# Kernel tuning notes

Measured on AMD Instinct MI355X. Metric: run time of the kernel, lower is better.

Reference implementation:

```python
import jax, jax.numpy as jnp
import numpy as np

ATTN_SPLITS = 2
TEMPERATURE = 10000.0

# ---------- split / merge helpers (faithful to split_feature / merge_splits) ----------

def split_cf(x, ns):  # channel-first [b,c,h,w] -> [b*ns*ns, c, h/ns, w/ns]
    b, c, h, w = x.shape
    x = x.reshape(b, c, ns, h // ns, ns, w // ns).transpose(0, 2, 4, 1, 3, 5)
    return x.reshape(b * ns * ns, c, h // ns, w // ns)

def merge_cf(x, ns):  # channel-first inverse
    b, c, h, w = x.shape
    nb = b // (ns * ns)
    x = x.reshape(nb, ns, ns, c, h, w).transpose(0, 3, 1, 4, 2, 5)
    return x.reshape(nb, c, ns * h, ns * w)

def split_cl(x, ns):  # channel-last [b,h,w,c] -> [b*ns*ns, h/ns, w/ns, c]
    b, h, w, c = x.shape
    x = x.reshape(b, ns, h // ns, ns, w // ns, c).transpose(0, 1, 3, 2, 4, 5)
    return x.reshape(b * ns * ns, h // ns, w // ns, c)

def merge_cl(x, ns):  # channel-last inverse
    b, h, w, c = x.shape
    nb = b // (ns * ns)
    x = x.reshape(nb, ns, ns, h, w, c).transpose(0, 1, 3, 2, 4, 5)
    return x.reshape(nb, ns * h, ns * w, c)

# ---------- PositionEmbeddingSine (normalize=True, scale=2*pi) ----------

def pos_embed_sine(h, w, num_pos_feats):
    scale = 2.0 * np.pi
    eps = 1e-6
    ones = jnp.ones((h, w), jnp.float32)
    y_embed = jnp.cumsum(ones, 0)
    x_embed = jnp.cumsum(ones, 1)
    y_embed = y_embed / (y_embed[-1:, :] + eps) * scale
    x_embed = x_embed / (x_embed[:, -1:] + eps) * scale
    dim_t = jnp.arange(num_pos_feats, dtype=jnp.float32)
    dim_t = TEMPERATURE ** (2.0 * jnp.floor(dim_t / 2.0) / num_pos_feats)
    pos_x = x_embed[:, :, None] / dim_t  # [h,w,npf]
    pos_y = y_embed[:, :, None] / dim_t
    pos_x = jnp.stack([jnp.sin(pos_x[:, :, 0::2]), jnp.cos(pos_x[:, :, 1::2])], -1).reshape(h, w, -1)
    pos_y = jnp.stack([jnp.sin(pos_y[:, :, 0::2]), jnp.cos(pos_y[:, :, 1::2])], -1).reshape(h, w, -1)
    pos = jnp.concatenate([pos_y, pos_x], -1)  # [h,w,c]
    return jnp.transpose(pos, (2, 0, 1))[None]  # [1,c,h,w]

def feature_add_position(f0, f1, attn_splits, c):
    if attn_splits > 1:
        f0s = split_cf(f0, attn_splits)
        f1s = split_cf(f1, attn_splits)
        pos = pos_embed_sine(f0s.shape[2], f0s.shape[3], c // 2)
        return merge_cf(f0s + pos, attn_splits), merge_cf(f1s + pos, attn_splits)
    pos = pos_embed_sine(f0.shape[2], f0.shape[3], c // 2)
    return f0 + pos, f1 + pos

# ---------- shifted-window attention mask (static, numpy) ----------

def shift_window_attn_mask(h, w, ns):
    wsh, wsw = h // ns, w // ns
    ssh, ssw = wsh // 2, wsw // 2
    img = np.zeros((h, w), np.float32)
    cnt = 0
    for hs in (slice(0, -wsh), slice(-wsh, -ssh), slice(-ssh, None)):
        for ws in (slice(0, -wsw), slice(-wsw, -ssw), slice(-ssw, None)):
            img[hs, ws] = cnt
            cnt += 1
    m = img.reshape(ns, wsh, ns, wsw).transpose(0, 2, 1, 3).reshape(ns * ns, wsh * wsw)
    am = m[:, None, :] - m[:, :, None]
    am = np.where(am != 0, -100.0, 0.0).astype(np.float32)
    return jnp.asarray(am)  # [ns*ns, N, N]

# ---------- single-head split (shifted) window attention ----------

def split_window_attention(q, k, v, ns, h, w, attn_mask):
    b, _, c = q.shape
    bn = b * ns * ns
    wsh, wsw = h // ns, w // ns
    ssh, ssw = wsh // 2, wsw // 2
    q = q.reshape(b, h, w, c)
    k = k.reshape(b, h, w, c)
    v = v.reshape(b, h, w, c)
    q = jnp.roll(q, (-ssh, -ssw), (1, 2))
    k = jnp.roll(k, (-ssh, -ssw), (1, 2))
    v = jnp.roll(v, (-ssh, -ssw), (1, 2))
    qs = split_cl(q, ns).reshape(bn, -1, c)
    ks = split_cl(k, ns).reshape(bn, -1, c)
    vs = split_cl(v, ns).reshape(bn, -1, c)
    scores = jnp.einsum('bnc,bmc->bnm', qs, ks) / jnp.sqrt(jnp.asarray(c, qs.dtype))
    scores = scores + jnp.tile(attn_mask, (b, 1, 1))
    attn = jax.nn.softmax(scores, axis=-1)
    out = jnp.einsum('bnm,bmc->bnc', attn, vs)
    out = merge_cl(out.reshape(bn, wsh, wsw, c), ns)
    out = jnp.roll(out, (ssh, ssw), (1, 2))
    return out.reshape(b, -1, c)

# ---------- global correlation softmax matching ----------

def global_correlation_softmax(f0, f1):
    b, c, h, w = f0.shape
    f0v = f0.reshape(b, c, -1)  # [b,c,hw]
    f1v = f1.reshape(b, c, -1)
    corr = jnp.einsum('bcn,bcm->bnm', f0v, f1v) / jnp.sqrt(jnp.asarray(c, f0.dtype))
    yy, xx = jnp.meshgrid(jnp.arange(h), jnp.arange(w), indexing='ij')
    grid = jnp.stack([xx, yy], 0).astype(f0.dtype)  # [2,h,w] (x,y)
    gridv = grid.reshape(2, -1).T  # [hw,2]
    prob = jax.nn.softmax(corr, axis=-1)
    corresp = jnp.einsum('bnm,md->bnd', prob, gridv).reshape(b, h, w, 2).transpose(0, 3, 1, 2)
    flow = corresp - grid[None]
    return flow

# ---------- setup & reference ----------

def setup_inputs() -> dict:
    key = jax.random.key(0)
    k0, k1 = jax.random.split(key)
    b, c, h, w = 4, 128, 64, 64
    feature0 = jax.random.normal(k0, (b, c, h, w), jnp.float32)
    feature1 = jax.random.normal(k1, (b, c, h, w), jnp.float32)
    return {'feature0': feature0, 'feature1': feature1}

def reference(feature0, feature1):
    b, c, h, w = feature0.shape
    ns = ATTN_SPLITS
    f0, f1 = feature_add_position(feature0, feature1, ns, c)
    attn_mask = shift_window_attn_mask(h, w, ns)
    q = f0.reshape(b, c, -1).transpose(0, 2, 1)  # [b,hw,c]
    kv = f1.reshape(b, c, -1).transpose(0, 2, 1)
    f0_attn = split_window_attention(q, kv, kv, ns, h, w, attn_mask)  # [b,hw,c]
    f0_attn = f0_attn.transpose(0, 2, 1).reshape(b, c, h, w)
    flow = global_correlation_softmax(f0_attn, f1)  # [b,2,h,w]
    return flow
```

## Files before the change

### kernel.cpp

```cpp
#include <hip/hip_runtime.h>
#include <hip/hip_bf16.h>
#include <math.h>

#define NB 4
#define NC 128
#define NH 64
#define NW 64
#define NHW 4096
#define SCALE 0.08838834764831845f

typedef short bf16x8 __attribute__((ext_vector_type(8)));
typedef float f32x4 __attribute__((ext_vector_type(4)));

__device__ __forceinline__ unsigned bfbits(float f) {
    unsigned u = __float_as_uint(f);
    return (u + 0x7FFFu + ((u >> 16) & 1u)) >> 16;
}
__device__ __forceinline__ unsigned bfpair(float a, float b) {
    return bfbits(a) | (bfbits(b) << 16);
}

__global__ __launch_bounds__(256) void pos_kernel(float* __restrict__ pos) {
    int idx = blockIdx.x * 256 + threadIdx.x;
    if (idx >= NC * 32 * 32) return;
    int x = idx & 31;
    int y = (idx >> 5) & 31;
    int c = idx >> 10;
    const float twopi = 6.283185307179586f;
    const float denom = 32.0f + 1e-6f;
    int cc = (c < 64) ? c : (c - 64);
    float e = (c < 64) ? (float)(y + 1) : (float)(x + 1);
    e = e * (twopi / denom);
    int k = cc >> 1;
    float arg = e * exp2f(-0.41524101186091903f * (float)k);
    pos[idx] = (cc & 1) ? cosf(arg) : sinf(arg);
}

__global__ __launch_bounds__(256) void pack_kernel(
        const float* __restrict__ f0, const float* __restrict__ f1,
        const float* __restrict__ pos,
        __hip_bfloat16* __restrict__ Qw, __hip_bfloat16* __restrict__ Kw,
        __hip_bfloat16* __restrict__ Bt, __hip_bfloat16* __restrict__ Ktw) {
    __shared__ float T[64][129];
    int blk = blockIdx.x;
    const bool isA = blk < 256;
    const float* src = isA ? f0 : f1;
    blk &= 255;
    const int y = blk & 63;
    const int b = blk >> 6;
    const int tid = threadIdx.x;
    const float* s = src + (size_t)b * NC * NHW + y * 64;
    for (int idx = tid; idx < 64 * NC; idx += 256) {
        const int x = idx & 63, c = idx >> 6;
        T[x][c] = s[c * NHW + x] + pos[(c << 10) + ((y & 31) << 5) + (x & 31)];
    }
    __syncthreads();
    const float sA = isA ? SCALE : 1.0f;
    const int yp = (y + 48) & 63;
    const int wi = yp >> 5, ry = yp & 31;
    for (int idx = tid; idx < 512; idx += 256) {
        const int x = idx >> 3, c0 = (idx & 7) * 16;
        const int xp = (x + 48) & 63;
        const int wj = xp >> 5, rx = xp & 31;
        const int win = b * 4 + wi * 2 + wj;
        const int tok = ry * 32 + rx;
        const float* tr = &T[x][c0];
        uint4 v0, v1;
        v0.x = bfpair(tr[0] * sA, tr[1] * sA);   v0.y = bfpair(tr[2] * sA, tr[3] * sA);
        v0.z = bfpair(tr[4] * sA, tr[5] * sA);   v0.w = bfpair(tr[6] * sA, tr[7] * sA);
        v1.x = bfpair(tr[8] * sA, tr[9] * sA);   v1.y = bfpair(tr[10] * sA, tr[11] * sA);
        v1.z = bfpair(tr[12] * sA, tr[13] * sA); v1.w = bfpair(tr[14] * sA, tr[15] * sA);
        __hip_bfloat16* wrow = (isA ? Qw : Kw) + ((size_t)win * 1024 + tok) * NC + c0;
        *reinterpret_cast<uint4*>(wrow) = v0;
        *reinterpret_cast<uint4*>(wrow + 8) = v1;
        if (!isA) {
            __hip_bfloat16* brow = Bt + ((size_t)b * NHW + y * 64 + x) * NC + c0;
            *reinterpret_cast<uint4*>(brow) = v0;
            *reinterpret_cast<uint4*>(brow + 8) = v1;
        }
    }
    if (!isA) {
        const int c = tid >> 1;
        const int wj = tid & 1;
        const int win = b * 4 + wi * 2 + wj;
        unsigned up[16];
        #pragma unroll
        for (int pr = 0; pr < 16; ++pr) {
            const int x0 = ((wj << 5) + 2 * pr + 16) & 63;
            up[pr] = bfpair(T[x0][c], T[x0 + 1][c]);
        }
        __hip_bfloat16* krow = Ktw + ((size_t)win * NC + c) * 1024 + ry * 32;
        uint4* uv = reinterpret_cast<uint4*>(up);
        #pragma unroll
        for (int i = 0; i < 4; ++i)
            *reinterpret_cast<uint4*>(krow + i * 8) = uv[i];
    }
}

__global__ __launch_bounds__(256) void attn_mfma_kernel(
        const __hip_bfloat16* __restrict__ Qw,
        const __hip_bfloat16* __restrict__ Kw,
        const __hip_bfloat16* __restrict__ Ktw,
        __hip_bfloat16* __restrict__ At) {
    __shared__ __align__(16) char lds[73728];
    char* KsB = lds;
    char* VsB = lds + 32768;
    char* Pscr = lds + 65536;
    const int tid = threadIdx.x;
    const int lane = tid & 63;
    const int w = tid >> 6;
    const int l15 = lane & 15;
    const int g = lane >> 4;
    const int blk = blockIdx.x;
    const int win = blk >> 4;
    const int qt = blk & 15;
    const int b = win >> 2, wi = (win >> 1) & 1, wj = win & 1;

    const char* Ksrc = (const char*)(Kw + (size_t)win * 1024 * NC);
    const char* Vsrc = (const char*)(Ktw + (size_t)win * NC * 1024);

    bf16x8 qf[4];
    {
        const __hip_bfloat16* qrow =
            Qw + ((size_t)win * 1024 + qt * 64 + w * 16 + l15) * NC + g * 8;
        #pragma unroll
        for (int kk = 0; kk < 4; ++kk)
            qf[kk] = *reinterpret_cast<const bf16x8*>(qrow + kk * 32);
    }

    const int reg_q = (wi ? (qt < 8 ? 1 : 2) : 0) * 3
                    + (wj ? ((w & 1) == 0 ? 1 : 2) : 0);

    auto stageK = [&](int buf, int kt) {
        const char* sb = Ksrc + (size_t)kt * 64 * 256;
        char* dst = KsB + buf * 16384;
        #pragma unroll
        for (int it = 0; it < 4; ++it) {
            const int obase = w * 4096 + it * 1024;
            const int o = obase + lane * 16;
            const int row = o >> 8;
            const int off = o & 255;
            __builtin_amdgcn_global_load_lds(
                (const __attribute__((address_space(1))) void*)(sb + row * 256 + (off ^ ((row & 7) << 4))),
                (__attribute__((address_space(3))) void*)(dst + obase), 16, 0, 0);
        }
    };
    auto stageV = [&](int buf, int kt) {
        char* dst = VsB + buf * 16384;
        #pragma unroll
        for (int it = 0; it < 4; ++it) {
            const int obase = w * 4096 + it * 1024;
            const int o = obase + lane * 16;
            const int crow = o >> 7;
            const int off = o & 127;
            __builtin_amdgcn_global_load_lds(
                (const __attribute__((address_space(1))) void*)(Vsrc + crow * 2048 + kt * 128 + (off ^ ((crow & 7) << 4))),
                (__attribute__((address_space(3))) void*)(dst + obase), 16, 0, 0);
        }
    };

    f32x4 oacc[8] = {{0,0,0,0},{0,0,0,0},{0,0,0,0},{0,0,0,0},
                     {0,0,0,0},{0,0,0,0},{0,0,0,0},{0,0,0,0}};
    float zacc = 0.f;

    stageK(0, 0); stageV(0, 0);
    __syncthreads();

    for (int kt = 0; kt < 16; ++kt) {
        const int buf = kt & 1;
        if (kt < 15) { stageK(buf ^ 1, kt + 1); stageV(buf ^ 1, kt + 1); }

        const char* kb = KsB + buf * 16384;
        f32x4 sacc[4] = {{0,0,0,0},{0,0,0,0},{0,0,0,0},{0,0,0,0}};
        #pragma unroll
        for (int kk = 0; kk < 4; ++kk) {
            #pragma unroll
            for (int msub = 0; msub < 4; ++msub) {
                const int byte = msub * 4096 + l15 * 256 + ((kk * 64 + g * 16) ^ ((l15 & 7) << 4));
                bf16x8 kf = *reinterpret_cast<const bf16x8*>(kb + byte);
                sacc[msub] = __builtin_amdgcn_mfma_f32_16x16x32_bf16(kf, qf[kk], sacc[msub], 0, 0, 0);
            }
        }

        const int rk_row = (wi ? (kt < 8 ? 1 : 2) : 0) * 3;
        char* pw = Pscr + w * 2048;
        #pragma unroll
        for (int msub = 0; msub < 4; ++msub) {
            const int rk = rk_row + (wj ? ((msub & 1) == 0 ? 1 : 2) : 0);
            const bool ok = (rk == reg_q);
            const float p0 = ok ? __expf(sacc[msub][0]) : 0.f;
            const float p1 = ok ? __expf(sacc[msub][1]) : 0.f;
            const float p2 = ok ? __expf(sacc[msub][2]) : 0.f;
            const float p3 = ok ? __expf(sacc[msub][3]) : 0.f;
            zacc += (p0 + p1) + (p2 + p3);
            *reinterpret_cast<unsigned*>(pw + l15 * 128 + ((msub * 32 + g * 8 + 0) ^ ((l15 & 7) << 4))) = bfpair(p0, p1);
            *reinterpret_cast<unsigned*>(pw + l15 * 128 + ((msub * 32 + g * 8 + 4) ^ ((l15 & 7) << 4))) = bfpair(p2, p3);
        }
        bf16x8 pf[2];
        #pragma unroll
        for (int kk = 0; kk < 2; ++kk)
            pf[kk] = *reinterpret_cast<const bf16x8*>(pw + l15 * 128 + ((kk * 64 + g * 16) ^ ((l15 & 7) << 4)));

        const char* vb = VsB + buf * 16384;
        #pragma unroll
        for (int kk = 0; kk < 2; ++kk) {
            #pragma unroll
            for (int co = 0; co < 8; ++co) {
                const int byte = (co * 16 + l15) * 128 + ((kk * 64 + g * 16) ^ ((l15 & 7) << 4));
                bf16x8 vf = *reinterpret_cast<const bf16x8*>(vb + byte);
                oacc[co] = __builtin_amdgcn_mfma_f32_16x16x32_bf16(pf[kk], vf, oacc[co], 0, 0, 0);
            }
        }
        __syncthreads();
    }

    float z = zacc;
    z += __shfl_xor(z, 16);
    z += __shfl_xor(z, 32);

    unsigned short* olds = reinterpret_cast<unsigned short*>(lds + w * 4096);
    #pragma unroll
    for (int r = 0; r < 4; ++r) {
        const float zi = SCALE / __shfl(z, g * 4 + r);
        #pragma unroll
        for (int co = 0; co < 8; ++co)
            olds[(g * 4 + r) * 128 + co * 16 + l15] = (unsigned short)bfbits(oacc[co][r] * zi);
    }

    const int qloc = lane >> 2;
    const int c0 = (lane & 3) * 32;
    const int tok = qt * 64 + w * 16 + qloc;
    const int yo = ((wi << 5) + (tok >> 5) + 16) & 63;
    const int xo = ((wj << 5) + (tok & 31) + 16) & 63;
    __hip_bfloat16* arow = At + ((size_t)b * NHW + yo * 64 + xo) * NC + c0;
    #pragma unroll
    for (int i = 0; i < 4; ++i) {
        int4 v = *reinterpret_cast<const int4*>(olds + qloc * 128 + c0 + i * 8);
        *reinterpret_cast<int4*>(arow + i * 8) = v;
    }
}

__global__ __launch_bounds__(256) void corr_part_kernel(
        const __hip_bfloat16* __restrict__ At,
        const __hip_bfloat16* __restrict__ Bt,
        float4* __restrict__ part) {
    __shared__ __hip_bfloat16 Bs[2][64 * 128];
    const int tid = threadIdx.x;
    const int lane = tid & 63;
    const int w = tid >> 6;
    const int blk = blockIdx.x;
    const int ms = blk & 3;
    const int nt = (blk >> 2) & 63;
    const int b = blk >> 8;
    const int l15 = lane & 15;
    const int g = lane >> 4;
    const int n0 = nt * 64;

    const __hip_bfloat16* Ab = At + (size_t)b * NHW * NC;
    const __hip_bfloat16* Bb = Bt + (size_t)b * NHW * NC;

    bf16x8 afrag[4];
    {
        const __hip_bfloat16* arow = Ab + (size_t)(n0 + w * 16 + l15) * NC + g * 8;
        #pragma unroll
        for (int kk = 0; kk < 4; ++kk)
            afrag[kk] = *reinterpret_cast<const bf16x8*>(arow + kk * 32);
    }

    auto stage = [&](int buf, int mtile) {
        const char* srcbase = reinterpret_cast<const char*>(Bb + (size_t)mtile * 64 * NC);
        #pragma unroll
        for (int it = 0; it < 4; ++it) {
            const int obase = w * 4096 + it * 1024;
            const int o = obase + lane * 16;
            const int row = o >> 8;
            const int off = o & 255;
            const char* src = srcbase + row * 256 + (off ^ ((row & 7) << 4));
            __builtin_amdgcn_global_load_lds(
                (const __attribute__((address_space(1))) void*)src,
                (__attribute__((address_space(3))) void*)((char*)&Bs[buf][0] + obase),
                16, 0, 0);
        }
    };

    f32x4 rl = {0, 0, 0, 0}, rsm = {0, 0, 0, 0}, rsy = {0, 0, 0, 0};

    stage(0, ms * 16);
    __syncthreads();

    for (int mt = 0; mt < 16; ++mt) {
        const int buf = mt & 1;
        if (mt < 15) stage(buf ^ 1, ms * 16 + mt + 1);

        f32x4 acc[4] = {{0,0,0,0},{0,0,0,0},{0,0,0,0},{0,0,0,0}};
        const char* base = (const char*)&Bs[buf][0];
        #pragma unroll
        for (int kk = 0; kk < 4; ++kk) {
            #pragma unroll
            for (int msub = 0; msub < 4; ++msub) {
                const int byte = msub * 4096 + l15 * 256 +
                                 ((kk * 64 + g * 16) ^ ((l15 & 7) << 4));
                bf16x8 bfrag = *reinterpret_cast<const bf16x8*>(base + byte);
                acc[msub] = __builtin_amdgcn_mfma_f32_16x16x32_bf16(
                    afrag[kk], bfrag, acc[msub], 0, 0, 0);
            }
        }
        const float y0 = (float)(ms * 16 + mt);
        #pragma unroll
        for (int r = 0; r < 4; ++r) {
            float p0 = __expf(acc[0][r]);
            float p1 = __expf(acc[1][r]);
            float p2 = __expf(acc[2][r]);
            float p3 = __expf(acc[3][r]);
            float ts = (p0 + p1) + (p2 + p3);
            rl[r]  += ts;
            rsy[r] += y0 * ts;
            rsm[r] += fmaf(3.f, p3, fmaf(2.f, p2, p1));
        }
        __syncthreads();
    }

    const float xl = (float)l15;
    #pragma unroll
    for (int r = 0; r < 4; ++r) {
        float a  = rl[r];
        float sx = xl * rl[r] + 16.f * rsm[r];
        float sy = rsy[r];
        #pragma unroll
        for (int m = 1; m < 16; m <<= 1) {
            a  += __shfl_xor(a, m);
            sx += __shfl_xor(sx, m);
            sy += __shfl_xor(sy, m);
        }
        if (l15 == 0) {
            const int n = n0 + w * 16 + g * 4 + r;
            part[((size_t)b * NHW + n) * 4 + ms] = make_float4(a, sx, sy, 0.f);
        }
    }
}

__global__ __launch_bounds__(256) void finalize_kernel(
        const float4* __restrict__ part, float* __restrict__ out) {
    const int idx = blockIdx.x * 256 + threadIdx.x;
    if (idx >= NB * NHW) return;
    const int n = idx & (NHW - 1);
    const int b = idx >> 12;
    float4 p0 = part[(size_t)idx * 4 + 0];
    float4 p1 = part[(size_t)idx * 4 + 1];
    float4 p2 = part[(size_t)idx * 4 + 2];
    float4 p3 = part[(size_t)idx * 4 + 3];
    const float l  = (p0.x + p1.x) + (p2.x + p3.x);
    const float sx = (p0.y + p1.y) + (p2.y + p3.y);
    const float sy = (p0.z + p1.z) + (p2.z + p3.z);
    const float inv = 1.0f / l;
    out[(size_t)b * 2 * NHW + n]       = sx * inv - (float)(n & 63);
    out[(size_t)b * 2 * NHW + NHW + n] = sy * inv - (float)(n >> 6);
}

extern "C" void kernel_launch(void* const* d_in, const int* in_sizes, int n_in,
                              void* d_out, int out_size, void* d_ws, size_t ws_size,
                              hipStream_t stream) {
    const float* f0 = (const float*)d_in[0];
    const float* f1 = (const float*)d_in[1];
    float* ws  = (float*)d_ws;
    float* pos = ws;
    __hip_bfloat16* Qw  = (__hip_bfloat16*)(pos + 131072);
    __hip_bfloat16* Kw  = Qw  + (size_t)16 * 1024 * NC;
    __hip_bfloat16* Bt  = Kw  + (size_t)16 * 1024 * NC;
    __hip_bfloat16* Ktw = Bt  + (size_t)NB * NHW * NC;
    __hip_bfloat16* At  = Ktw + (size_t)16 * NC * 1024;
    float4* part = (float4*)(At + (size_t)NB * NHW * NC);
    float* out = (float*)d_out;

    pos_kernel<<<512, 256, 0, stream>>>(pos);
    pack_kernel<<<512, 256, 0, stream>>>(f0, f1, pos, Qw, Kw, Bt, Ktw);
    attn_mfma_kernel<<<256, 256, 0, stream>>>(Qw, Kw, Ktw, At);
    corr_part_kernel<<<1024, 256, 0, stream>>>(At, Bt, part);
    finalize_kernel<<<64, 256, 0, stream>>>(part, out);
}
```

Before: 70.12 us.

## Inline position embedding, drop windowed Q/K copies, reshape correlation tiling

The separate position-embedding kernel is removed and sin/cos is computed inline in the pack kernel. The windowed, shifted Q and K buffers are no longer written; the attention kernel gathers Q and K rows directly from the plain row-major layouts using shifted-window index math, which saves one launch and two full bf16 copies. The correlation kernel now gives each wave 32 query rows sharing the staged B tile, with 8 M-splits instead of 4, and finalize sums 8 partials. This trades extra transcendental work in pack and scattered K loads for less global traffic and more reuse of each B tile.

Measured after the change: 74.75 us. +6.6%, slower.

```diff
diff --git a/kernel.cpp b/kernel.cpp
--- a/kernel.cpp
+++ b/kernel.cpp
@@ -20,27 +20,19 @@
     return bfbits(a) | (bfbits(b) << 16);
 }
 
-__global__ __launch_bounds__(256) void pos_kernel(float* __restrict__ pos) {
-    int idx = blockIdx.x * 256 + threadIdx.x;
-    if (idx >= NC * 32 * 32) return;
-    int x = idx & 31;
-    int y = (idx >> 5) & 31;
-    int c = idx >> 10;
-    const float twopi = 6.283185307179586f;
-    const float denom = 32.0f + 1e-6f;
-    int cc = (c < 64) ? c : (c - 64);
-    float e = (c < 64) ? (float)(y + 1) : (float)(x + 1);
-    e = e * (twopi / denom);
-    int k = cc >> 1;
-    float arg = e * exp2f(-0.41524101186091903f * (float)k);
-    pos[idx] = (cc & 1) ? cosf(arg) : sinf(arg);
+__device__ __forceinline__ float posval(int c, int yy, int xx) {
+    const float twopi_over_denom = 6.283185307179586f / (32.0f + 1e-6f);
+    const int cc = (c < 64) ? c : (c - 64);
+    const float e = (float)(((c < 64) ? yy : xx) + 1) * twopi_over_denom;
+    const int k = cc >> 1;
+    const float arg = e * exp2f(-0.41524101186091903f * (float)k);
+    return (cc & 1) ? cosf(arg) : sinf(arg);
 }
 
 __global__ __launch_bounds__(256) void pack_kernel(
         const float* __restrict__ f0, const float* __restrict__ f1,
-        const float* __restrict__ pos,
-        __hip_bfloat16* __restrict__ Qw, __hip_bfloat16* __restrict__ Kw,
-        __hip_bfloat16* __restrict__ Bt, __hip_bfloat16* __restrict__ Ktw) {
+        __hip_bfloat16* __restrict__ F0t, __hip_bfloat16* __restrict__ Bt,
+        __hip_bfloat16* __restrict__ Ktw) {
     __shared__ float T[64][129];
     int blk = blockIdx.x;
     const bool isA = blk < 256;
@@ -50,36 +42,28 @@
     const int b = blk >> 6;
     const int tid = threadIdx.x;
     const float* s = src + (size_t)b * NC * NHW + y * 64;
+    const float sA = isA ? SCALE : 1.0f;
     for (int idx = tid; idx < 64 * NC; idx += 256) {
         const int x = idx & 63, c = idx >> 6;
-        T[x][c] = s[c * NHW + x] + pos[(c << 10) + ((y & 31) << 5) + (x & 31)];
+        T[x][c] = (s[c * NHW + x] + posval(c, y & 31, x & 31)) * sA;
     }
     __syncthreads();
-    const float sA = isA ? SCALE : 1.0f;
-    const int yp = (y + 48) & 63;
-    const int wi = yp >> 5, ry = yp & 31;
+    __hip_bfloat16* dst = isA ? F0t : Bt;
     for (int idx = tid; idx < 512; idx += 256) {
         const int x = idx >> 3, c0 = (idx & 7) * 16;
-        const int xp = (x + 48) & 63;
-        const int wj = xp >> 5, rx = xp & 31;
-        const int win = b * 4 + wi * 2 + wj;
-        const int tok = ry * 32 + rx;
         const float* tr = &T[x][c0];
         uint4 v0, v1;
-        v0.x = bfpair(tr[0] * sA, tr[1] * sA);   v0.y = bfpair(tr[2] * sA, tr[3] * sA);
-        v0.z = bfpair(tr[4] * sA, tr[5] * sA);   v0.w = bfpair(tr[6] * sA, tr[7] * sA);
-        v1.x = bfpair(tr[8] * sA, tr[9] * sA);   v1.y = bfpair(tr[10] * sA, tr[11] * sA);
-        v1.z = bfpair(tr[12] * sA, tr[13] * sA); v1.w = bfpair(tr[14] * sA, tr[15] * sA);
-        __hip_bfloat16* wrow = (isA ? Qw : Kw) + ((size_t)win * 1024 + tok) * NC + c0;
-        *reinterpret_cast<uint4*>(wrow) = v0;
-        *reinterpret_cast<uint4*>(wrow + 8) = v1;
-        if (!isA) {
-            __hip_bfloat16* brow = Bt + ((size_t)b * NHW + y * 64 + x) * NC + c0;
-            *reinterpret_cast<uint4*>(brow) = v0;
-            *reinterpret_cast<uint4*>(brow + 8) = v1;
-        }
+        v0.x = bfpair(tr[0], tr[1]);   v0.y = bfpair(tr[2], tr[3]);
+        v0.z = bfpair(tr[4], tr[5]);   v0.w = bfpair(tr[6], tr[7]);
+        v1.x = bfpair(tr[8], tr[9]);   v1.y = bfpair(tr[10], tr[11]);
+        v1.z = bfpair(tr[12], tr[13]); v1.w = bfpair(tr[14], tr[15]);
+        __hip_bfloat16* row = dst + ((size_t)b * NHW + y * 64 + x) * NC + c0;
+        *reinterpret_cast<uint4*>(row) = v0;
+        *reinterpret_cast<uint4*>(row + 8) = v1;
     }
     if (!isA) {
+        const int yp = (y + 48) & 63;
+        const int wi = yp >> 5, ry = yp & 31;
         const int c = tid >> 1;
         const int wj = tid & 1;
         const int win = b * 4 + wi * 2 + wj;
@@ -98,8 +82,8 @@
 }
 
 __global__ __launch_bounds__(256) void attn_mfma_kernel(
-        const __hip_bfloat16* __restrict__ Qw,
-        const __hip_bfloat16* __restrict__ Kw,
+        const __hip_bfloat16* __restrict__ F0t,
+        const __hip_bfloat16* __restrict__ Bt,
         const __hip_bfloat16* __restrict__ Ktw,
         __hip_bfloat16* __restrict__ At) {
     __shared__ __align__(16) char lds[73728];
@@ -116,13 +100,16 @@
     const int qt = blk & 15;
     const int b = win >> 2, wi = (win >> 1) & 1, wj = win & 1;
 
-    const char* Ksrc = (const char*)(Kw + (size_t)win * 1024 * NC);
+    const char* Btb = (const char*)(Bt + (size_t)b * NHW * NC);
     const char* Vsrc = (const char*)(Ktw + (size_t)win * NC * 1024);
 
     bf16x8 qf[4];
     {
+        const int tok = qt * 64 + w * 16 + l15;
+        const int yo = ((wi << 5) + (tok >> 5) + 16) & 63;
+        const int xo = ((wj << 5) + (tok & 31) + 16) & 63;
         const __hip_bfloat16* qrow =
-            Qw + ((size_t)win * 1024 + qt * 64 + w * 16 + l15) * NC + g * 8;
+            F0t + ((size_t)b * NHW + yo * 64 + xo) * NC + g * 8;
         #pragma unroll
         for (int kk = 0; kk < 4; ++kk)
             qf[kk] = *reinterpret_cast<const bf16x8*>(qrow + kk * 32);
@@ -132,16 +119,18 @@
                     + (wj ? ((w & 1) == 0 ? 1 : 2) : 0);
 
     auto stageK = [&](int buf, int kt) {
-        const char* sb = Ksrc + (size_t)kt * 64 * 256;
         char* dst = KsB + buf * 16384;
         #pragma unroll
         for (int it = 0; it < 4; ++it) {
             const int obase = w * 4096 + it * 1024;
-            const int o = obase + lane * 16;
-            const int row = o >> 8;
-            const int off = o & 255;
+            const int row = w * 16 + it * 4 + (lane >> 4);
+            const int tok = kt * 64 + row;
+            const int yo = ((wi << 5) + (tok >> 5) + 16) & 63;
+            const int xo = ((wj << 5) + (tok & 31) + 16) & 63;
+            const char* src = Btb + (yo * 64 + xo) * 256 +
+                              (((lane & 15) * 16) ^ ((row & 7) << 4));
             __builtin_amdgcn_global_load_lds(
-                (const __attribute__((address_space(1))) void*)(sb + row * 256 + (off ^ ((row & 7) << 4))),
+                (const __attribute__((address_space(1))) void*)src,
                 (__attribute__((address_space(3))) void*)(dst + obase), 16, 0, 0);
         }
     };
@@ -249,22 +238,23 @@
     const int lane = tid & 63;
     const int w = tid >> 6;
     const int blk = blockIdx.x;
-    const int ms = blk & 3;
-    const int nt = (blk >> 2) & 63;
+    const int ms = blk & 7;
+    const int nt = (blk >> 3) & 31;
     const int b = blk >> 8;
     const int l15 = lane & 15;
     const int g = lane >> 4;
-    const int n0 = nt * 64;
+    const int n0 = nt * 128 + w * 32;
 
     const __hip_bfloat16* Ab = At + (size_t)b * NHW * NC;
     const __hip_bfloat16* Bb = Bt + (size_t)b * NHW * NC;
 
-    bf16x8 afrag[4];
-    {
-        const __hip_bfloat16* arow = Ab + (size_t)(n0 + w * 16 + l15) * NC + g * 8;
+    bf16x8 afrag[2][4];
+    #pragma unroll
+    for (int s = 0; s < 2; ++s) {
+        const __hip_bfloat16* arow = Ab + (size_t)(n0 + s * 16 + l15) * NC + g * 8;
         #pragma unroll
         for (int kk = 0; kk < 4; ++kk)
-            afrag[kk] = *reinterpret_cast<const bf16x8*>(arow + kk * 32);
+            afrag[s][kk] = *reinterpret_cast<const bf16x8*>(arow + kk * 32);
     }
 
     auto stage = [&](int buf, int mtile) {
@@ -283,16 +273,19 @@
         }
     };
 
-    f32x4 rl = {0, 0, 0, 0}, rsm = {0, 0, 0, 0}, rsy = {0, 0, 0, 0};
-
-    stage(0, ms * 16);
+    f32x4 rl[2] = {{0,0,0,0},{0,0,0,0}};
+    f32x4 rsm[2] = {{0,0,0,0},{0,0,0,0}};
+    f32x4 rsy[2] = {{0,0,0,0},{0,0,0,0}};
+
+    stage(0, ms * 8);
     __syncthreads();
 
-    for (int mt = 0; mt < 16; ++mt) {
+    for (int mt = 0; mt < 8; ++mt) {
         const int buf = mt & 1;
-        if (mt < 15) stage(buf ^ 1, ms * 16 + mt + 1);
-
-        f32x4 acc[4] = {{0,0,0,0},{0,0,0,0},{0,0,0,0},{0,0,0,0}};
+        if (mt < 7) stage(buf ^ 1, ms * 8 + mt + 1);
+
+        f32x4 acc[2][4] = {{{0,0,0,0},{0,0,0,0},{0,0,0,0},{0,0,0,0}},
+                           {{0,0,0,0},{0,0,0,0},{0,0,0,0},{0,0,0,0}}};
         const char* base = (const char*)&Bs[buf][0];
         #pragma unroll
         for (int kk = 0; kk < 4; ++kk) {
@@ -301,40 +294,48 @@
                 const int byte = msub * 4096 + l15 * 256 +
                                  ((kk * 64 + g * 16) ^ ((l15 & 7) << 4));
                 bf16x8 bfrag = *reinterpret_cast<const bf16x8*>(base + byte);
-                acc[msub] = __builtin_amdgcn_mfma_f32_16x16x32_bf16(
-                    afrag[kk], bfrag, acc[msub], 0, 0, 0);
-            }
-        }
-        const float y0 = (float)(ms * 16 + mt);
+                acc[0][msub] = __builtin_amdgcn_mfma_f32_16x16x32_bf16(
+                    afrag[0][kk], bfrag, acc[0][msub], 0, 0, 0);
+                acc[1][msub] = __builtin_amdgcn_mfma_f32_16x16x32_bf16(
+                    afrag[1][kk], bfrag, acc[1][msub], 0, 0, 0);
+            }
+        }
+        const float y0 = (float)(ms * 8 + mt);
+        #pragma unroll
+        for (int s = 0; s < 2; ++s) {
+            #pragma unroll
+            for (int r = 0; r < 4; ++r) {
+                float p0 = __expf(acc[s][0][r]);
+                float p1 = __expf(acc[s][1][r]);
+                float p2 = __expf(acc[s][2][r]);
+                float p3 = __expf(acc[s][3][r]);
+                float ts = (p0 + p1) + (p2 + p3);
+                rl[s][r]  += ts;
+                rsy[s][r] += y0 * ts;
+                rsm[s][r] += fmaf(3.f, p3, fmaf(2.f, p2, p1));
+            }
+        }
+        __syncthreads();
+    }
+
+    const float xl = (float)l15;
+    #pragma unroll
+    for (int s = 0; s < 2; ++s) {
         #pragma unroll
         for (int r = 0; r < 4; ++r) {
-            float p0 = __expf(acc[0][r]);
-            float p1 = __expf(acc[1][r]);
-            float p2 = __expf(acc[2][r]);
-            float p3 = __expf(acc[3][r]);
-            float ts = (p0 + p1) + (p2 + p3);
-            rl[r]  += ts;
-            rsy[r] += y0 * ts;
-            rsm[r] += fmaf(3.f, p3, fmaf(2.f, p2, p1));
-        }
-        __syncthreads();
-    }
-
-    const float xl = (float)l15;
-    #pragma unroll
-    for (int r = 0; r < 4; ++r) {
-        float a  = rl[r];
-        float sx = xl * rl[r] + 16.f * rsm[r];
-        float sy = rsy[r];
-        #pragma unroll
-        for (int m = 1; m < 16; m <<= 1) {
-            a  += __shfl_xor(a, m);
-            sx += __shfl_xor(sx, m);
-            sy += __shfl_xor(sy, m);
-        }
-        if (l15 == 0) {
-            const int n = n0 + w * 16 + g * 4 + r;
-            part[((size_t)b * NHW + n) * 4 + ms] = make_float4(a, sx, sy, 0.f);
+            float a  = rl[s][r];
+            float sx = xl * rl[s][r] + 16.f * rsm[s][r];
+            float sy = rsy[s][r];
+            #pragma unroll
+            for (int m = 1; m < 16; m <<= 1) {
+                a  += __shfl_xor(a, m);
+                sx += __shfl_xor(sx, m);
+                sy += __shfl_xor(sy, m);
+            }
+            if (l15 == 0) {
+                const int n = n0 + s * 16 + g * 4 + r;
+                part[((size_t)b * NHW + n) * 8 + ms] = make_float4(a, sx, sy, 0.f);
+            }
         }
     }
 }
@@ -345,13 +346,12 @@
     if (idx >= NB * NHW) return;
     const int n = idx & (NHW - 1);
     const int b = idx >> 12;
-    float4 p0 = part[(size_t)idx * 4 + 0];
-    float4 p1 = part[(size_t)idx * 4 + 1];
-    float4 p2 = part[(size_t)idx * 4 + 2];
-    float4 p3 = part[(size_t)idx * 4 + 3];
-    const float l  = (p0.x + p1.x) + (p2.x + p3.x);
-    const float sx = (p0.y + p1.y) + (p2.y + p3.y);
-    const float sy = (p0.z + p1.z) + (p2.z + p3.z);
+    float l = 0.f, sx = 0.f, sy = 0.f;
+    #pragma unroll
+    for (int i = 0; i < 8; ++i) {
+        float4 p = part[(size_t)idx * 8 + i];
+        l += p.x; sx += p.y; sy += p.z;
+    }
     const float inv = 1.0f / l;
     out[(size_t)b * 2 * NHW + n]       = sx * inv - (float)(n & 63);
     out[(size_t)b * 2 * NHW + NHW + n] = sy * inv - (float)(n >> 6);
@@ -362,19 +362,15 @@
                               hipStream_t stream) {
     const float* f0 = (const float*)d_in[0];
     const float* f1 = (const float*)d_in[1];
-    float* ws  = (float*)d_ws;
-    float* pos = ws;
-    __hip_bfloat16* Qw  = (__hip_bfloat16*)(pos + 131072);
-    __hip_bfloat16* Kw  = Qw  + (size_t)16 * 1024 * NC;
-    __hip_bfloat16* Bt  = Kw  + (size_t)16 * 1024 * NC;
+    __hip_bfloat16* F0t = (__hip_bfloat16*)d_ws;
+    __hip_bfloat16* Bt  = F0t + (size_t)NB * NHW * NC;
     __hip_bfloat16* Ktw = Bt  + (size_t)NB * NHW * NC;
     __hip_bfloat16* At  = Ktw + (size_t)16 * NC * 1024;
     float4* part = (float4*)(At + (size_t)NB * NHW * NC);
     float* out = (float*)d_out;
 
-    pos_kernel<<<512, 256, 0, stream>>>(pos);
-    pack_kernel<<<512, 256, 0, stream>>>(f0, f1, pos, Qw, Kw, Bt, Ktw);
-    attn_mfma_kernel<<<256, 256, 0, stream>>>(Qw, Kw, Ktw, At);
+    pack_kernel<<<512, 256, 0, stream>>>(f0, f1, F0t, Bt, Ktw);
+    attn_mfma_kernel<<<256, 256, 0, stream>>>(F0t, Bt, Ktw, At);
     corr_part_kernel<<<1024, 256, 0, stream>>>(At, Bt, part);
     finalize_kernel<<<64, 256, 0, stream>>>(part, out);
 }
```
